# Performance work log

Hardware: AMD Instinct MI355X
Metric: run time of the kernel (lower is better)

The kernel has to match this reference:

```python
import jax, jax.numpy as jnp
import numpy as np

N, B, D_IN, UNITS, K = 8192, 1, 2, 64, 2
F = D_IN + UNITS        # concatenated feature size per node
M = K + 1               # number of diffusion matrices (x0..xK)


def setup_inputs() -> dict:
    key = jax.random.key(0)
    k1, k2, k3, k4, k5, k6 = jax.random.split(key, 6)
    inputs = jax.random.normal(k1, (B, N * D_IN), dtype=jnp.float32)
    hx = jax.random.normal(k2, (B, N * UNITS), dtype=jnp.float32)
    adj = jax.random.uniform(k3, (N, N), dtype=jnp.float32)
    w_ru = jax.random.normal(k4, (F * M, 2 * UNITS), dtype=jnp.float32) * (2.0 / (F * M + 2 * UNITS)) ** 0.5
    b_ru = jnp.ones((2 * UNITS,), dtype=jnp.float32)  # bias_start=1.0 for gates
    w_c = jax.random.normal(k5, (F * M, UNITS), dtype=jnp.float32) * (2.0 / (F * M + UNITS)) ** 0.5
    b_c = jnp.zeros((UNITS,), dtype=jnp.float32)
    node_index = jax.random.randint(k6, (N,), 0, N)
    return {"inputs": inputs, "hx": hx, "adj": adj, "w_ru": w_ru,
            "b_ru": b_ru, "w_c": w_c, "b_c": b_c, "node_index": node_index}


def _gconv(adj_mx, inp, state, W, b, out_size):
    # inp: [B, N, D_IN], state: [B, N, UNITS]
    x = jnp.concatenate([inp, state], axis=2)              # [B, N, F]
    x0 = jnp.transpose(x, (1, 2, 0)).reshape(N, F * B)     # [N, F*B]
    xs = [x0]
    x1 = adj_mx @ x0                                       # 1-hop diffusion
    xs.append(x1)
    for _ in range(2, K + 1):                              # Chebyshev-style recurrence
        x2 = 2.0 * (adj_mx @ x1) - x0
        xs.append(x2)
        x0, x1 = x1, x2
    xk = jnp.stack(xs, 0).reshape(M, N, F, B)              # [M, N, F, B]
    xk = jnp.transpose(xk, (3, 1, 2, 0)).reshape(B * N, F * M)
    out = xk @ W + b                                       # [B*N, out_size]
    return out.reshape(B, N * out_size)


def reference(inputs, hx, adj, w_ru, b_ru, w_c, b_c, node_index):
    # square adj branch: adj_mx = ((D^-1)(A+I))^T, d_mat_inv = I (unused)
    adj2 = adj + jnp.eye(N, dtype=adj.dtype)
    d_inv = 1.0 / jnp.sum(adj2, axis=1)                    # no inf: diagonal added
    adj_mx = (adj2 * d_inv[:, None]).T
    inp = inputs.reshape(B, N, D_IN)
    h3 = hx.reshape(B, N, UNITS)
    value = jax.nn.sigmoid(_gconv(adj_mx, inp, h3, w_ru, b_ru, 2 * UNITS))
    value = value.reshape(B, N, 2 * UNITS)
    r = value[..., :UNITS].reshape(B, N * UNITS)
    u = value[..., UNITS:].reshape(B, N * UNITS)
    c = jnp.tanh(_gconv(adj_mx, inp, (r * hx).reshape(B, N, UNITS), w_c, b_c, UNITS))
    new_state = u * hx + (1.0 - u) * c                     # [B, N*UNITS]
    return new_state
```

## Files before the change

### kernel.cpp

```cpp
#include <hip/hip_runtime.h>
#include <math.h>


typedef __attribute__((ext_vector_type(4))) float f32x4;
typedef __attribute__((ext_vector_type(2))) int v2i;
typedef __attribute__((ext_vector_type(4))) int v4i;
typedef unsigned char uch;

constexpr int NN  = 8192;
constexpr int CST = 80;
constexpr int KBT = 256;
constexpr int SFT = KBT / 2;
constexpr int MCH = 4;
constexpr size_t NS    = (size_t)NN * CST;
constexpr size_t UTFS8 = (size_t)SFT * 5 * 1024;

constexpr float SC1  = 4096.f,   ISC1 = 1.f / 4096.f;
constexpr float SC2  = 262144.f, ISC2 = 1.f / 262144.f;

static __device__ __forceinline__ unsigned f2e4m3(float x) {
  union { float f; unsigned u; } c; c.f = x;
  unsigned s = (c.u >> 24) & 0x80u;
  float a = fabsf(x);
  if (a >= 464.f) return s | 0x7Eu;
  if (a < 0.015625f) {
    int q = (int)(a * 512.f + 0.5f);
    return s | (unsigned)q;
  }
  c.f = a;
  unsigned u = c.u + (0x7FFFFu + ((c.u >> 20) & 1u));
  int e = (int)((u >> 23) & 0xFFu) - 127;
  unsigned m = (u >> 20) & 7u;
  if (e > 8) return s | 0x7Eu;
  return s | (unsigned)(((e + 7) << 3) | m);
}

static __device__ __forceinline__ void mfma_f8(f32x4& acc, v2i a, v2i b) {
  asm("v_mfma_f32_16x16x32_fp8_fp8 %0, %1, %2, %0" : "+v"(acc) : "v"(a), "v"(b));
}
static __device__ __forceinline__ v2i lo2(v4i v) { v2i r; r.x = v.x; r.y = v.y; return r; }
static __device__ __forceinline__ v2i hi2(v4i v) { v2i r; r.x = v.z; r.y = v.w; return r; }

__global__ __launch_bounds__(256, 4) void k_conv(const float* __restrict__ adj,
                                                 uch* __restrict__ adjF8,
                                                 float* __restrict__ dpart) {
  __shared__ float tile[2][32][132];
  const int kb = blockIdx.x, mc = blockIdx.y;
  const int tid = threadIdx.x;
  const int l = tid & 63, w = tid >> 6;
  const int rg = tid >> 5;
  const int cb = (tid & 31) * 4;
  const float* src = adj + ((size_t)kb * 32 + rg) * NN + (size_t)mc * 2048 + cb;
  float rs[4] = {0.f, 0.f, 0.f, 0.f};
  float4 vA[4], vB[4];

#pragma unroll
  for (int i = 0; i < 4; ++i)
    vA[i] = *(const float4*)(src + (size_t)(8 * i) * NN);

#define CONV_BODY(CH, BUF, VC, VN)                                             \
  {                                                                            \
    const int ch_ = (CH);                                                      \
    _Pragma("unroll") for (int i = 0; i < 4; ++i) {                            \
      int r = rg + 8 * i;                                                      \
      int colp = (cb + 8 * i) & 127;                                           \
      *(float4*)&tile[BUF][r][colp] = VC[i];                                   \
      rs[i] += (VC[i].x + VC[i].y) + (VC[i].z + VC[i].w);                      \
    }                                                                          \
    if (ch_ < 15) {                                                            \
      _Pragma("unroll") for (int i = 0; i < 4; ++i)                            \
          VN[i] = *(const float4*)(src + (size_t)(8 * i) * NN + (ch_ + 1) * 128); \
    }                                                                          \
    __syncthreads();                                                           \
    _Pragma("unroll") for (int h = 0; h < 2; ++h) {                            \
      int fl = w + 4 * h;                                                      \
      int mt = mc * 128 + ch_ * 8 + fl;                                        \
      int colp = (fl * 16 + (l & 15) + 8 * (l >> 4)) & 127;                    \
      unsigned plo = 0, phi = 0;                                               \
      _Pragma("unroll") for (int j = 0; j < 4; ++j)                            \
        plo |= f2e4m3(tile[BUF][8 * (l >> 4) + j][colp]) << (8 * j);           \
      _Pragma("unroll") for (int j = 4; j < 8; ++j)                            \
        phi |= f2e4m3(tile[BUF][8 * (l >> 4) + j][colp]) << (8 * (j - 4));     \
      uint2 pk; pk.x = plo; pk.y = phi;                                        \
      *(uint2*)(adjF8 + ((size_t)mt * SFT + (kb >> 1)) * 1024                  \
                + l * 16 + (kb & 1) * 8) = pk;                                 \
    }                                                                          \
  }

  for (int cp = 0; cp < 8; ++cp) {
    CONV_BODY(2 * cp,     0, vA, vB);
    CONV_BODY(2 * cp + 1, 1, vB, vA);
  }
#undef CONV_BODY

#pragma unroll
  for (int i = 0; i < 4; ++i) {
#pragma unroll
    for (int m = 16; m >= 1; m >>= 1) rs[i] += __shfl_xor(rs[i], m);
  }
  if ((tid & 31) == 0) {
#pragma unroll
    for (int i = 0; i < 4; ++i)
      dpart[(size_t)mc * NN + kb * 32 + 8 * i + rg] = rs[i];
  }
}

__global__ __launch_bounds__(256) void k_build(const float* __restrict__ hx,
                                               const float* __restrict__ inp,
                                               const float* __restrict__ dpart,
                                               float* __restrict__ dinv,
                                               float* __restrict__ X0,
                                               float* __restrict__ XS0,
                                               uch* __restrict__ UtF8) {
  __shared__ float dv_s[32];
  const int bid = blockIdx.x;
  const int n0 = bid * 32;
  const int tid = threadIdx.x;
  if (tid < 32) {
    int n = n0 + tid;
    float dv = 1.f / (dpart[n] + dpart[NN + n] + dpart[2 * NN + n] +
                      dpart[3 * NN + n] + 1.f);
    dv_s[tid] = dv;
    dinv[n] = dv;
  }
  __syncthreads();
  for (int p = tid; p < 32 * 20; p += 256) {
    int nl = p / 20, c4 = (p % 20) * 4;
    int n = n0 + nl;
    float dv = dv_s[nl];
    float v[4];
#pragma unroll
    for (int j = 0; j < 4; ++j) {
      int c = c4 + j;
      v[j] = (c < 64) ? hx[n * 64 + c] : (c < 66 ? inp[n * 2 + (c - 64)] : 0.f);
    }
    size_t o = (size_t)n * CST + c4;
    *(float4*)(X0 + o)  = make_float4(v[0], v[1], v[2], v[3]);
    *(float4*)(XS0 + o) = make_float4(dv * v[0], dv * v[1], dv * v[2], dv * v[3]);
  }
  for (int p = tid; p < 5 * 64; p += 256) {
    int nt = p >> 6, l = p & 63;
    unsigned plo = 0, phi = 0;
#pragma unroll
    for (int j = 0; j < 8; ++j) {
      int nloc = 8 * (l >> 4) + j;
      int n = n0 + nloc;
      int c = nt * 16 + (l & 15);
      float v = (c < 64) ? hx[n * 64 + c] : (c < 66 ? inp[n * 2 + (c - 64)] : 0.f);
      unsigned b = f2e4m3(v * dv_s[nloc] * SC1);
      if (j < 4) plo |= b << (8 * j); else phi |= b << (8 * (j - 4));
    }
    uint2 pk; pk.x = plo; pk.y = phi;
    *(uint2*)(UtF8 + ((size_t)(bid >> 1) * 5 + nt) * 1024 + l * 16 + (bid & 1) * 8) = pk;
  }
}

static __device__ __forceinline__ void gemm_core2(const uch* __restrict__ adjF8,
                                                  const uch* __restrict__ bF8,
                                                  int bid, int tid, float* smem,
                                                  float sv[5], float inv_scale) {
  const int w8 = tid >> 6, l = tid & 63;
  const int sf0 = w8 * 16;
  f32x4 acc0[5], acc1[5];
#pragma unroll
  for (int nt = 0; nt < 5; ++nt) {
    acc0[nt] = (f32x4){0.f, 0.f, 0.f, 0.f};
    acc1[nt] = (f32x4){0.f, 0.f, 0.f, 0.f};
  }
  const uch* ap = adjF8 + ((size_t)(2 * bid) * SFT + sf0) * 1024 + l * 16;
  const size_t MSTR = (size_t)SFT * 1024;
  const uch* bp = bF8 + (size_t)sf0 * 5 * 1024 + l * 16;

  v4i A0e, A1e, A0o, A1o, Be[5], Bo[5];
  A0e = *(const v4i*)(ap);
  A1e = *(const v4i*)(ap + MSTR);
#pragma unroll
  for (int nt = 0; nt < 5; ++nt) Be[nt] = *(const v4i*)(bp + nt * 1024);

  for (int sf = 0; sf < 16; sf += 2) {
    A0o = *(const v4i*)(ap + (size_t)(sf + 1) * 1024);
    A1o = *(const v4i*)(ap + MSTR + (size_t)(sf + 1) * 1024);
#pragma unroll
    for (int nt = 0; nt < 5; ++nt)
      Bo[nt] = *(const v4i*)(bp + (size_t)((sf + 1) * 5 + nt) * 1024);
#pragma unroll
    for (int nt = 0; nt < 5; ++nt) {
      mfma_f8(acc0[nt], lo2(A0e), lo2(Be[nt]));
      mfma_f8(acc1[nt], lo2(A1e), lo2(Be[nt]));
    }
#pragma unroll
    for (int nt = 0; nt < 5; ++nt) {
      mfma_f8(acc0[nt], hi2(A0e), hi2(Be[nt]));
      mfma_f8(acc1[nt], hi2(A1e), hi2(Be[nt]));
    }
    A0e = *(const v4i*)(ap + (size_t)(sf + 2) * 1024);
    A1e = *(const v4i*)(ap + MSTR + (size_t)(sf + 2) * 1024);
#pragma unroll
    for (int nt = 0; nt < 5; ++nt)
      Be[nt] = *(const v4i*)(bp + (size_t)((sf + 2) * 5 + nt) * 1024);
#pragma unroll
    for (int nt = 0; nt < 5; ++nt) {
      mfma_f8(acc0[nt], lo2(A0o), lo2(Bo[nt]));
      mfma_f8(acc1[nt], lo2(A1o), lo2(Bo[nt]));
    }
#pragma unroll
    for (int nt = 0; nt < 5; ++nt) {
      mfma_f8(acc0[nt], hi2(A0o), hi2(Bo[nt]));
      mfma_f8(acc1[nt], hi2(A1o), hi2(Bo[nt]));
    }
  }
  asm volatile("s_nop 7\n\ts_nop 7\n\ts_nop 7" ::: "memory");

  auto red = reinterpret_cast<float(*)[64][40]>(smem);
  if (w8 < 4) {
#pragma unroll
    for (int nt = 0; nt < 5; ++nt) {
      *(f32x4*)&red[w8][l][nt * 4]      = acc0[nt];
      *(f32x4*)&red[w8][l][20 + nt * 4] = acc1[nt];
    }
  }
  __syncthreads();
  if (w8 >= 4) {
#pragma unroll
    for (int nt = 0; nt < 5; ++nt) {
      f32x4 t0 = *(f32x4*)&red[w8 - 4][l][nt * 4];
      f32x4 t1 = *(f32x4*)&red[w8 - 4][l][20 + nt * 4];
      *(f32x4*)&red[w8 - 4][l][nt * 4]      = t0 + acc0[nt];
      *(f32x4*)&red[w8 - 4][l][20 + nt * 4] = t1 + acc1[nt];
    }
  }
  __syncthreads();
#pragma unroll
  for (int i = 0; i < 5; ++i) {
    int p = tid + i * 512;
    int r = p / 80, c = p % 80;
    int mtl = r >> 4, rl = r & 15;
    int ll = ((rl >> 2) << 4) | (c & 15);
    int slot = mtl * 20 + (((c >> 4) << 2) | (rl & 3));
    sv[i] = (((red[0][ll][slot] + red[1][ll][slot]) +
              red[2][ll][slot]) + red[3][ll][slot]) * inv_scale;
  }
  __syncthreads();
}

__global__ __launch_bounds__(512, 1) void k_hop1(const uch* __restrict__ adjF8,
                                                 const uch* __restrict__ UtFin,
                                                 const float* __restrict__ XSin,
                                                 const float* __restrict__ dinv,
                                                 float* __restrict__ X1,
                                                 float* __restrict__ XS1,
                                                 uch* __restrict__ UtFout) {
  __shared__ __align__(16) float smem[10240];
  const int bid = blockIdx.x, tid = threadIdx.x;
  const int n0 = bid * 32;
  float sv[5];
  gemm_core2(adjF8, UtFin, bid, tid, smem, sv, ISC1);

  auto xs = reinterpret_cast<float(*)[80]>(smem);
#pragma unroll
  for (int i = 0; i < 5; ++i) {
    int p = tid + i * 512;
    size_t o = (size_t)n0 * CST + p;
    float x1 = XSin[o] + sv[i];
    X1[o] = x1;
    float z = dinv[n0 + p / 80] * x1;
    XS1[o] = z;
    xs[p / 80][p % 80] = z;
  }
  __syncthreads();
  for (int p = tid; p < 5 * 64; p += 512) {
    int nt = p >> 6, l = p & 63;
    unsigned plo = 0, phi = 0;
#pragma unroll
    for (int j = 0; j < 8; ++j) {
      unsigned b = f2e4m3(xs[8 * (l >> 4) + j][nt * 16 + (l & 15)] * SC2);
      if (j < 4) plo |= b << (8 * j); else phi |= b << (8 * (j - 4));
    }
    uint2 pk; pk.x = plo; pk.y = phi;
    *(uint2*)(UtFout + ((size_t)(bid >> 1) * 5 + nt) * 1024 + l * 16 + (bid & 1) * 8) = pk;
  }
}

__global__ __launch_bounds__(512, 1) void k_hop2g(const uch* __restrict__ adjF8,
    const uch* __restrict__ UtFb, const float* __restrict__ XS1,
    const float* __restrict__ X0, const float* __restrict__ X1,
    const float* __restrict__ w_ru, const float* __restrict__ b_ru,
    const float* __restrict__ hx, const float* __restrict__ inp,
    const float* __restrict__ dinv,
    float* __restrict__ X0w, float* __restrict__ XS0w,
    uch* __restrict__ UtFa, float* __restrict__ UG) {
  __shared__ __align__(16) float smem[10240];
  const int bid = blockIdx.x, tid = threadIdx.x;
  const int n0 = bid * 32;
  float sv[5];
  gemm_core2(adjF8, UtFb, bid, tid, smem, sv, ISC2);

  auto xr2 = reinterpret_cast<float(*)[80]>(smem);
  float* xr01 = smem + 2560;
  float* rhq  = smem + 2560 + 4352;
#pragma unroll
  for (int i = 0; i < 5; ++i) {
    int p = tid + i * 512;
    size_t o = (size_t)n0 * CST + p;
    xr2[p / 80][p % 80] = 2.f * (XS1[o] + sv[i]) - X0[o];
  }
  for (int p = tid; p < 32 * 17; p += 512) {
    int nl = p / 17, c4 = (p % 17) * 4;
    size_t o = (size_t)(n0 + nl) * CST + c4;
    *(float4*)&xr01[nl * 68 + c4]            = *(const float4*)(X0 + o);
    *(float4*)&xr01[32 * 68 + nl * 68 + c4]  = *(const float4*)(X1 + o);
  }
  __syncthreads();

  const int nl = tid >> 4, og = tid & 15, o0 = og * 8;
  float acc[8];
#pragma unroll
  for (int j = 0; j < 8; ++j) acc[j] = b_ru[o0 + j];
  for (int c = 0; c < 66; ++c) {
    int f = (c < 64) ? (c + 2) : (c - 64);
    const float* wr = w_ru + (size_t)(f * 3) * 128 + o0;
    float xv[3];
    xv[0] = xr01[nl * 68 + c];
    xv[1] = xr01[32 * 68 + nl * 68 + c];
    xv[2] = xr2[nl][c];
#pragma unroll
    for (int m = 0; m < 3; ++m) {
      float wl[8];
      *(float4*)(wl)     = *(const float4*)(wr + m * 128);
      *(float4*)(wl + 4) = *(const float4*)(wr + m * 128 + 4);
#pragma unroll
      for (int j = 0; j < 8; ++j) acc[j] += xv[m] * wl[j];
    }
  }
  const int n = n0 + nl;
  const float dv = dinv[n];
  if (og < 8) {
#pragma unroll
    for (int j = 0; j < 8; ++j) {
      int o = o0 + j;
      float r = 1.f / (1.f + expf(-acc[j]));
      float rh = r * hx[n * 64 + o];
      X0w[(size_t)n * CST + o] = rh;
      float srh = dv * rh;
      XS0w[(size_t)n * CST + o] = srh;
      rhq[nl * 64 + o] = srh;
    }
  } else {
#pragma unroll
    for (int j = 0; j < 8; ++j)
      UG[n * 64 + (o0 - 64) + j] = 1.f / (1.f + expf(-acc[j]));
  }
  __syncthreads();
  for (int p = tid; p < 5 * 64; p += 512) {
    int nt = p >> 6, l = p & 63;
    unsigned plo = 0, phi = 0;
#pragma unroll
    for (int j = 0; j < 8; ++j) {
      int lr = 8 * (l >> 4) + j;
      int nn = n0 + lr;
      int c = nt * 16 + (l & 15);
      float v;
      if (c < 64)      v = rhq[lr * 64 + c];
      else if (c < 66) v = dinv[nn] * inp[nn * 2 + (c - 64)];
      else             v = 0.f;
      unsigned b = f2e4m3(v * SC1);
      if (j < 4) plo |= b << (8 * j); else phi |= b << (8 * (j - 4));
    }
    uint2 pk; pk.x = plo; pk.y = phi;
    *(uint2*)(UtFa + ((size_t)(bid >> 1) * 5 + nt) * 1024 + l * 16 + (bid & 1) * 8) = pk;
  }
}

__global__ __launch_bounds__(512, 1) void k_hop2f(const uch* __restrict__ adjF8,
    const uch* __restrict__ UtFb, const float* __restrict__ XS1,
    const float* __restrict__ X0, const float* __restrict__ X1,
    const float* __restrict__ w_c, const float* __restrict__ b_c,
    const float* __restrict__ hx, const float* __restrict__ UG,
    float* __restrict__ out) {
  __shared__ __align__(16) float smem[10240];
  const int bid = blockIdx.x, tid = threadIdx.x;
  const int n0 = bid * 32;
  float sv[5];
  gemm_core2(adjF8, UtFb, bid, tid, smem, sv, ISC2);

  auto xr2 = reinterpret_cast<float(*)[80]>(smem);
  float* xr01 = smem + 2560;
#pragma unroll
  for (int i = 0; i < 5; ++i) {
    int p = tid + i * 512;
    size_t o = (size_t)n0 * CST + p;
    xr2[p / 80][p % 80] = 2.f * (XS1[o] + sv[i]) - X0[o];
  }
  for (int p = tid; p < 32 * 17; p += 512) {
    int nl = p / 17, c4 = (p % 17) * 4;
    size_t o = (size_t)(n0 + nl) * CST + c4;
    *(float4*)&xr01[nl * 68 + c4]           = *(const float4*)(X0 + o);
    *(float4*)&xr01[32 * 68 + nl * 68 + c4] = *(const float4*)(X1 + o);
  }
  __syncthreads();

  const int nl = tid >> 4, ot = tid & 15, o0 = ot * 4;
  float acc[4];
#pragma unroll
  for (int j = 0; j < 4; ++j) acc[j] = b_c[o0 + j];
  for (int c = 0; c < 66; ++c) {
    int f = (c < 64) ? (c + 2) : (c - 64);
    float xv[3];
    xv[0] = xr01[nl * 68 + c];
    xv[1] = xr01[32 * 68 + nl * 68 + c];
    xv[2] = xr2[nl][c];
#pragma unroll
    for (int m = 0; m < 3; ++m) {
      float wl[4];
      *(float4*)(wl) = *(const float4*)(w_c + (size_t)(f * 3 + m) * 64 + o0);
#pragma unroll
      for (int j = 0; j < 4; ++j) acc[j] += xv[m] * wl[j];
    }
  }
  const int n = n0 + nl;
#pragma unroll
  for (int j = 0; j < 4; ++j) {
    int o = o0 + j;
    float cc = tanhf(acc[j]);
    float u = UG[n * 64 + o];
    float h = hx[n * 64 + o];
    out[n * 64 + o] = u * h + (1.f - u) * cc;
  }
}

extern "C" void kernel_launch(void* const* d_in, const int* in_sizes, int n_in,
                              void* d_out, int out_size, void* d_ws, size_t ws_size,
                              hipStream_t stream) {
  const float* inp  = (const float*)d_in[0];
  const float* hx   = (const float*)d_in[1];
  const float* adj  = (const float*)d_in[2];
  const float* w_ru = (const float*)d_in[3];
  const float* b_ru = (const float*)d_in[4];
  const float* w_c  = (const float*)d_in[5];
  const float* b_c  = (const float*)d_in[6];
  float* out = (float*)d_out;

  float* ws    = (float*)d_ws;
  float* dinv  = ws;
  float* dpart = ws + 8192;
  float* X0    = ws + 8192 + 4 * 8192;
  float* XS0   = X0 + NS;
  float* X1    = XS0 + NS;
  float* XS1   = X1 + NS;
  uch* UtFa8   = (uch*)(XS1 + NS);
  uch* UtFb8   = UtFa8 + UTFS8;
  uch* adjF8   = UtFb8 + UTFS8;
  float* UG    = (float*)(adjF8 + (size_t)512 * SFT * 1024);

  dim3 cg(KBT, MCH);

  k_conv <<<cg, 256, 0, stream>>>(adj, adjF8, dpart);
  k_build<<<NN / 32, 256, 0, stream>>>(hx, inp, dpart, dinv, X0, XS0, UtFa8);

  k_hop1 <<<256, 512, 0, stream>>>(adjF8, UtFa8, XS0, dinv, X1, XS1, UtFb8);
  k_hop2g<<<256, 512, 0, stream>>>(adjF8, UtFb8, XS1, X0, X1, w_ru, b_ru, hx, inp,
                                   dinv, X0, XS0, UtFa8, UG);

  k_hop1 <<<256, 512, 0, stream>>>(adjF8, UtFa8, XS0, dinv, X1, XS1, UtFb8);
  k_hop2f<<<256, 512, 0, stream>>>(adjF8, UtFb8, XS1, X0, X1, w_c, b_c, hx, UG, out);
}
```

Baseline: 228.5 us.

## Fuse build and hop kernels into one cooperative kernel with bf16 intermediates

Replaces the build, two hop1 and two hop2 launches with one cooperative kernel that uses grid-wide syncs between phases, which removes per-launch overhead and tail gaps. Intermediate feature matrices are stored as bf16 instead of fp32, and the scaled copies XS0/XS1 are dropped and recomputed from dinv, which cuts global memory traffic. The software fp8 conversion is replaced by the hardware packed-convert instruction. In exchange, grid.sync adds synchronisation cost, bf16 storage lowers intermediate precision, and the hardware convert may round or saturate differently.

Result: slower. 308.5 us (+35.0%).

```diff
diff --git a/kernel.cpp b/kernel.cpp
--- a/kernel.cpp
+++ b/kernel.cpp
@@ -1,11 +1,15 @@
 #include <hip/hip_runtime.h>
+#include <hip/hip_cooperative_groups.h>
 #include <math.h>
+
+namespace cg = cooperative_groups;
 
 
 typedef __attribute__((ext_vector_type(4))) float f32x4;
 typedef __attribute__((ext_vector_type(2))) int v2i;
 typedef __attribute__((ext_vector_type(4))) int v4i;
 typedef unsigned char uch;
+typedef unsigned short ush;
 
 constexpr int NN  = 8192;
 constexpr int CST = 80;
@@ -18,21 +22,26 @@
 constexpr float SC1  = 4096.f,   ISC1 = 1.f / 4096.f;
 constexpr float SC2  = 262144.f, ISC2 = 1.f / 262144.f;
 
-static __device__ __forceinline__ unsigned f2e4m3(float x) {
+static __device__ __forceinline__ float bf2f(ush u) {
+  union { float f; unsigned v; } c; c.v = ((unsigned)u) << 16; return c.f;
+}
+static __device__ __forceinline__ ush f2bf(float x) {
   union { float f; unsigned u; } c; c.f = x;
-  unsigned s = (c.u >> 24) & 0x80u;
-  float a = fabsf(x);
-  if (a >= 464.f) return s | 0x7Eu;
-  if (a < 0.015625f) {
-    int q = (int)(a * 512.f + 0.5f);
-    return s | (unsigned)q;
-  }
-  c.f = a;
-  unsigned u = c.u + (0x7FFFFu + ((c.u >> 20) & 1u));
-  int e = (int)((u >> 23) & 0xFFu) - 127;
-  unsigned m = (u >> 20) & 7u;
-  if (e > 8) return s | 0x7Eu;
-  return s | (unsigned)(((e + 7) << 3) | m);
+  unsigned u = c.u;
+  u += 0x7fffu + ((u >> 16) & 1u);
+  return (ush)(u >> 16);
+}
+
+static __device__ __forceinline__ unsigned cvt2_fp8(float a, float b) {
+  unsigned r = 0;
+  asm("v_cvt_pk_fp8_f32 %0, %1, %2" : "+v"(r) : "v"(a), "v"(b));
+  return r;
+}
+static __device__ __forceinline__ uint2 pack8_fp8(const float* tv) {
+  uint2 pk;
+  pk.x = cvt2_fp8(tv[0], tv[1]) | (cvt2_fp8(tv[2], tv[3]) << 16);
+  pk.y = cvt2_fp8(tv[4], tv[5]) | (cvt2_fp8(tv[6], tv[7]) << 16);
+  return pk;
 }
 
 static __device__ __forceinline__ void mfma_f8(f32x4& acc, v2i a, v2i b) {
@@ -76,12 +85,10 @@
       int fl = w + 4 * h;                                                      \
       int mt = mc * 128 + ch_ * 8 + fl;                                        \
       int colp = (fl * 16 + (l & 15) + 8 * (l >> 4)) & 127;                    \
-      unsigned plo = 0, phi = 0;                                               \
-      _Pragma("unroll") for (int j = 0; j < 4; ++j)                            \
-        plo |= f2e4m3(tile[BUF][8 * (l >> 4) + j][colp]) << (8 * j);           \
-      _Pragma("unroll") for (int j = 4; j < 8; ++j)                            \
-        phi |= f2e4m3(tile[BUF][8 * (l >> 4) + j][colp]) << (8 * (j - 4));     \
-      uint2 pk; pk.x = plo; pk.y = phi;                                        \
+      float tv[8];                                                             \
+      _Pragma("unroll") for (int j = 0; j < 8; ++j)                            \
+        tv[j] = tile[BUF][8 * (l >> 4) + j][colp];                             \
+      uint2 pk = pack8_fp8(tv);                                                \
       *(uint2*)(adjF8 + ((size_t)mt * SFT + (kb >> 1)) * 1024                  \
                 + l * 16 + (kb & 1) * 8) = pk;                                 \
     }                                                                          \
@@ -102,56 +109,6 @@
 #pragma unroll
     for (int i = 0; i < 4; ++i)
       dpart[(size_t)mc * NN + kb * 32 + 8 * i + rg] = rs[i];
-  }
-}
-
-__global__ __launch_bounds__(256) void k_build(const float* __restrict__ hx,
-                                               const float* __restrict__ inp,
-                                               const float* __restrict__ dpart,
-                                               float* __restrict__ dinv,
-                                               float* __restrict__ X0,
-                                               float* __restrict__ XS0,
-                                               uch* __restrict__ UtF8) {
-  __shared__ float dv_s[32];
-  const int bid = blockIdx.x;
-  const int n0 = bid * 32;
-  const int tid = threadIdx.x;
-  if (tid < 32) {
-    int n = n0 + tid;
-    float dv = 1.f / (dpart[n] + dpart[NN + n] + dpart[2 * NN + n] +
-                      dpart[3 * NN + n] + 1.f);
-    dv_s[tid] = dv;
-    dinv[n] = dv;
-  }
-  __syncthreads();
-  for (int p = tid; p < 32 * 20; p += 256) {
-    int nl = p / 20, c4 = (p % 20) * 4;
-    int n = n0 + nl;
-    float dv = dv_s[nl];
-    float v[4];
-#pragma unroll
-    for (int j = 0; j < 4; ++j) {
-      int c = c4 + j;
-      v[j] = (c < 64) ? hx[n * 64 + c] : (c < 66 ? inp[n * 2 + (c - 64)] : 0.f);
-    }
-    size_t o = (size_t)n * CST + c4;
-    *(float4*)(X0 + o)  = make_float4(v[0], v[1], v[2], v[3]);
-    *(float4*)(XS0 + o) = make_float4(dv * v[0], dv * v[1], dv * v[2], dv * v[3]);
-  }
-  for (int p = tid; p < 5 * 64; p += 256) {
-    int nt = p >> 6, l = p & 63;
-    unsigned plo = 0, phi = 0;
-#pragma unroll
-    for (int j = 0; j < 8; ++j) {
-      int nloc = 8 * (l >> 4) + j;
-      int n = n0 + nloc;
-      int c = nt * 16 + (l & 15);
-      float v = (c < 64) ? hx[n * 64 + c] : (c < 66 ? inp[n * 2 + (c - 64)] : 0.f);
-      unsigned b = f2e4m3(v * dv_s[nloc] * SC1);
-      if (j < 4) plo |= b << (8 * j); else phi |= b << (8 * (j - 4));
-    }
-    uint2 pk; pk.x = plo; pk.y = phi;
-    *(uint2*)(UtF8 + ((size_t)(bid >> 1) * 5 + nt) * 1024 + l * 16 + (bid & 1) * 8) = pk;
   }
 }
 
@@ -167,8 +124,8 @@
     acc0[nt] = (f32x4){0.f, 0.f, 0.f, 0.f};
     acc1[nt] = (f32x4){0.f, 0.f, 0.f, 0.f};
   }
+  const size_t MSTR = (size_t)SFT * 1024;
   const uch* ap = adjF8 + ((size_t)(2 * bid) * SFT + sf0) * 1024 + l * 16;
-  const size_t MSTR = (size_t)SFT * 1024;
   const uch* bp = bF8 + (size_t)sf0 * 5 * 1024 + l * 16;
 
   v4i A0e, A1e, A0o, A1o, Be[5], Bo[5];
@@ -243,188 +200,219 @@
   __syncthreads();
 }
 
-__global__ __launch_bounds__(512, 1) void k_hop1(const uch* __restrict__ adjF8,
-                                                 const uch* __restrict__ UtFin,
-                                                 const float* __restrict__ XSin,
-                                                 const float* __restrict__ dinv,
-                                                 float* __restrict__ X1,
-                                                 float* __restrict__ XS1,
-                                                 uch* __restrict__ UtFout) {
+__global__ __launch_bounds__(512, 2) void k_mega(
+    const float* __restrict__ hx, const float* __restrict__ inp,
+    const float* __restrict__ w_ru, const float* __restrict__ b_ru,
+    const float* __restrict__ w_c, const float* __restrict__ b_c,
+    float* __restrict__ out,
+    const float* __restrict__ dpart, float* __restrict__ dinv,
+    ush* __restrict__ X0b, ush* __restrict__ X1b,
+    uch* __restrict__ UtFa8, uch* __restrict__ UtFb8,
+    const uch* __restrict__ adjF8, float* __restrict__ UG) {
+  cg::grid_group grid = cg::this_grid();
   __shared__ __align__(16) float smem[10240];
-  const int bid = blockIdx.x, tid = threadIdx.x;
-  const int n0 = bid * 32;
-  float sv[5];
-  gemm_core2(adjF8, UtFin, bid, tid, smem, sv, ISC1);
-
-  auto xs = reinterpret_cast<float(*)[80]>(smem);
-#pragma unroll
-  for (int i = 0; i < 5; ++i) {
-    int p = tid + i * 512;
-    size_t o = (size_t)n0 * CST + p;
-    float x1 = XSin[o] + sv[i];
-    X1[o] = x1;
-    float z = dinv[n0 + p / 80] * x1;
-    XS1[o] = z;
-    xs[p / 80][p % 80] = z;
-  }
-  __syncthreads();
-  for (int p = tid; p < 5 * 64; p += 512) {
-    int nt = p >> 6, l = p & 63;
-    unsigned plo = 0, phi = 0;
-#pragma unroll
-    for (int j = 0; j < 8; ++j) {
-      unsigned b = f2e4m3(xs[8 * (l >> 4) + j][nt * 16 + (l & 15)] * SC2);
-      if (j < 4) plo |= b << (8 * j); else phi |= b << (8 * (j - 4));
-    }
-    uint2 pk; pk.x = plo; pk.y = phi;
-    *(uint2*)(UtFout + ((size_t)(bid >> 1) * 5 + nt) * 1024 + l * 16 + (bid & 1) * 8) = pk;
-  }
-}
-
-__global__ __launch_bounds__(512, 1) void k_hop2g(const uch* __restrict__ adjF8,
-    const uch* __restrict__ UtFb, const float* __restrict__ XS1,
-    const float* __restrict__ X0, const float* __restrict__ X1,
-    const float* __restrict__ w_ru, const float* __restrict__ b_ru,
-    const float* __restrict__ hx, const float* __restrict__ inp,
-    const float* __restrict__ dinv,
-    float* __restrict__ X0w, float* __restrict__ XS0w,
-    uch* __restrict__ UtFa, float* __restrict__ UG) {
-  __shared__ __align__(16) float smem[10240];
-  const int bid = blockIdx.x, tid = threadIdx.x;
-  const int n0 = bid * 32;
-  float sv[5];
-  gemm_core2(adjF8, UtFb, bid, tid, smem, sv, ISC2);
-
-  auto xr2 = reinterpret_cast<float(*)[80]>(smem);
-  float* xr01 = smem + 2560;
-  float* rhq  = smem + 2560 + 4352;
-#pragma unroll
-  for (int i = 0; i < 5; ++i) {
-    int p = tid + i * 512;
-    size_t o = (size_t)n0 * CST + p;
-    xr2[p / 80][p % 80] = 2.f * (XS1[o] + sv[i]) - X0[o];
-  }
-  for (int p = tid; p < 32 * 17; p += 512) {
-    int nl = p / 17, c4 = (p % 17) * 4;
-    size_t o = (size_t)(n0 + nl) * CST + c4;
-    *(float4*)&xr01[nl * 68 + c4]            = *(const float4*)(X0 + o);
-    *(float4*)&xr01[32 * 68 + nl * 68 + c4]  = *(const float4*)(X1 + o);
-  }
-  __syncthreads();
-
-  const int nl = tid >> 4, og = tid & 15, o0 = og * 8;
-  float acc[8];
-#pragma unroll
-  for (int j = 0; j < 8; ++j) acc[j] = b_ru[o0 + j];
-  for (int c = 0; c < 66; ++c) {
-    int f = (c < 64) ? (c + 2) : (c - 64);
-    const float* wr = w_ru + (size_t)(f * 3) * 128 + o0;
-    float xv[3];
-    xv[0] = xr01[nl * 68 + c];
-    xv[1] = xr01[32 * 68 + nl * 68 + c];
-    xv[2] = xr2[nl][c];
-#pragma unroll
-    for (int m = 0; m < 3; ++m) {
-      float wl[8];
-      *(float4*)(wl)     = *(const float4*)(wr + m * 128);
-      *(float4*)(wl + 4) = *(const float4*)(wr + m * 128 + 4);
-#pragma unroll
-      for (int j = 0; j < 8; ++j) acc[j] += xv[m] * wl[j];
-    }
-  }
-  const int n = n0 + nl;
-  const float dv = dinv[n];
-  if (og < 8) {
-#pragma unroll
-    for (int j = 0; j < 8; ++j) {
-      int o = o0 + j;
-      float r = 1.f / (1.f + expf(-acc[j]));
-      float rh = r * hx[n * 64 + o];
-      X0w[(size_t)n * CST + o] = rh;
-      float srh = dv * rh;
-      XS0w[(size_t)n * CST + o] = srh;
-      rhq[nl * 64 + o] = srh;
-    }
-  } else {
-#pragma unroll
-    for (int j = 0; j < 8; ++j)
-      UG[n * 64 + (o0 - 64) + j] = 1.f / (1.f + expf(-acc[j]));
-  }
-  __syncthreads();
-  for (int p = tid; p < 5 * 64; p += 512) {
-    int nt = p >> 6, l = p & 63;
-    unsigned plo = 0, phi = 0;
-#pragma unroll
-    for (int j = 0; j < 8; ++j) {
-      int lr = 8 * (l >> 4) + j;
-      int nn = n0 + lr;
-      int c = nt * 16 + (l & 15);
-      float v;
-      if (c < 64)      v = rhq[lr * 64 + c];
-      else if (c < 66) v = dinv[nn] * inp[nn * 2 + (c - 64)];
-      else             v = 0.f;
-      unsigned b = f2e4m3(v * SC1);
-      if (j < 4) plo |= b << (8 * j); else phi |= b << (8 * (j - 4));
-    }
-    uint2 pk; pk.x = plo; pk.y = phi;
-    *(uint2*)(UtFa + ((size_t)(bid >> 1) * 5 + nt) * 1024 + l * 16 + (bid & 1) * 8) = pk;
-  }
-}
-
-__global__ __launch_bounds__(512, 1) void k_hop2f(const uch* __restrict__ adjF8,
-    const uch* __restrict__ UtFb, const float* __restrict__ XS1,
-    const float* __restrict__ X0, const float* __restrict__ X1,
-    const float* __restrict__ w_c, const float* __restrict__ b_c,
-    const float* __restrict__ hx, const float* __restrict__ UG,
-    float* __restrict__ out) {
-  __shared__ __align__(16) float smem[10240];
-  const int bid = blockIdx.x, tid = threadIdx.x;
-  const int n0 = bid * 32;
-  float sv[5];
-  gemm_core2(adjF8, UtFb, bid, tid, smem, sv, ISC2);
-
-  auto xr2 = reinterpret_cast<float(*)[80]>(smem);
-  float* xr01 = smem + 2560;
-#pragma unroll
-  for (int i = 0; i < 5; ++i) {
-    int p = tid + i * 512;
-    size_t o = (size_t)n0 * CST + p;
-    xr2[p / 80][p % 80] = 2.f * (XS1[o] + sv[i]) - X0[o];
-  }
-  for (int p = tid; p < 32 * 17; p += 512) {
-    int nl = p / 17, c4 = (p % 17) * 4;
-    size_t o = (size_t)(n0 + nl) * CST + c4;
-    *(float4*)&xr01[nl * 68 + c4]           = *(const float4*)(X0 + o);
-    *(float4*)&xr01[32 * 68 + nl * 68 + c4] = *(const float4*)(X1 + o);
-  }
-  __syncthreads();
-
-  const int nl = tid >> 4, ot = tid & 15, o0 = ot * 4;
-  float acc[4];
-#pragma unroll
-  for (int j = 0; j < 4; ++j) acc[j] = b_c[o0 + j];
-  for (int c = 0; c < 66; ++c) {
-    int f = (c < 64) ? (c + 2) : (c - 64);
-    float xv[3];
-    xv[0] = xr01[nl * 68 + c];
-    xv[1] = xr01[32 * 68 + nl * 68 + c];
-    xv[2] = xr2[nl][c];
-#pragma unroll
-    for (int m = 0; m < 3; ++m) {
-      float wl[4];
-      *(float4*)(wl) = *(const float4*)(w_c + (size_t)(f * 3 + m) * 64 + o0);
-#pragma unroll
-      for (int j = 0; j < 4; ++j) acc[j] += xv[m] * wl[j];
-    }
-  }
-  const int n = n0 + nl;
-#pragma unroll
-  for (int j = 0; j < 4; ++j) {
-    int o = o0 + j;
-    float cc = tanhf(acc[j]);
-    float u = UG[n * 64 + o];
-    float h = hx[n * 64 + o];
-    out[n * 64 + o] = u * h + (1.f - u) * cc;
+  const int b = blockIdx.x, tid = threadIdx.x;
+  const int n0 = b * 32;
+
+  {
+    float* dv_s = smem;
+    if (tid < 32) {
+      int n = n0 + tid;
+      float dv = 1.f / (dpart[n] + dpart[NN + n] + dpart[2 * NN + n] +
+                        dpart[3 * NN + n] + 1.f);
+      dv_s[tid] = dv;
+      dinv[n] = dv;
+    }
+    __syncthreads();
+    for (int p = tid; p < 32 * 20; p += 512) {
+      int nl = p / 20, c4 = (p % 20) * 4;
+      int n = n0 + nl;
+      float v[4];
+#pragma unroll
+      for (int j = 0; j < 4; ++j) {
+        int c = c4 + j;
+        v[j] = (c < 64) ? hx[n * 64 + c] : (c < 66 ? inp[n * 2 + (c - 64)] : 0.f);
+      }
+      uint2 pk;
+      pk.x = f2bf(v[0]) | ((unsigned)f2bf(v[1]) << 16);
+      pk.y = f2bf(v[2]) | ((unsigned)f2bf(v[3]) << 16);
+      *(uint2*)(X0b + (size_t)n * CST + c4) = pk;
+    }
+    for (int p = tid; p < 5 * 64; p += 512) {
+      int nt = p >> 6, l = p & 63;
+      float tv[8];
+#pragma unroll
+      for (int j = 0; j < 8; ++j) {
+        int lr = 8 * (l >> 4) + j;
+        int n = n0 + lr;
+        int c = nt * 16 + (l & 15);
+        float v = (c < 64) ? hx[n * 64 + c] : (c < 66 ? inp[n * 2 + (c - 64)] : 0.f);
+        tv[j] = v * dv_s[lr] * SC1;
+      }
+      uint2 pk = pack8_fp8(tv);
+      *(uint2*)(UtFa8 + ((size_t)(b >> 1) * 5 + nt) * 1024 + l * 16 + (b & 1) * 8) = pk;
+    }
+  }
+  grid.sync();
+
+#pragma unroll 1
+  for (int round = 0; round < 2; ++round) {
+    {
+      float sv[5];
+      gemm_core2(adjF8, UtFa8, b, tid, smem, sv, ISC1);
+      auto xs = reinterpret_cast<float(*)[80]>(smem);
+#pragma unroll
+      for (int i = 0; i < 5; ++i) {
+        int p = tid + i * 512;
+        size_t o = (size_t)n0 * CST + p;
+        float dv = dinv[n0 + p / 80];
+        float x1 = dv * bf2f(X0b[o]) + sv[i];
+        X1b[o] = f2bf(x1);
+        xs[p / 80][p % 80] = dv * x1;
+      }
+      __syncthreads();
+      for (int p = tid; p < 5 * 64; p += 512) {
+        int nt = p >> 6, l = p & 63;
+        float tv[8];
+#pragma unroll
+        for (int j = 0; j < 8; ++j)
+          tv[j] = xs[8 * (l >> 4) + j][nt * 16 + (l & 15)] * SC2;
+        uint2 pk = pack8_fp8(tv);
+        *(uint2*)(UtFb8 + ((size_t)(b >> 1) * 5 + nt) * 1024 + l * 16 + (b & 1) * 8) = pk;
+      }
+    }
+    grid.sync();
+
+    if (round == 0) {
+      float sv[5];
+      gemm_core2(adjF8, UtFb8, b, tid, smem, sv, ISC2);
+      auto xr2 = reinterpret_cast<float(*)[80]>(smem);
+      float* xr01 = smem + 2560;
+      float* rhq  = smem + 2560 + 4352;
+#pragma unroll
+      for (int i = 0; i < 5; ++i) {
+        int p = tid + i * 512;
+        size_t o = (size_t)n0 * CST + p;
+        float dv = dinv[n0 + p / 80];
+        xr2[p / 80][p % 80] = 2.f * (dv * bf2f(X1b[o]) + sv[i]) - bf2f(X0b[o]);
+      }
+      for (int p = tid; p < 32 * 17; p += 512) {
+        int nl = p / 17, c4 = (p % 17) * 4;
+        size_t o = (size_t)(n0 + nl) * CST + c4;
+#pragma unroll
+        for (int j = 0; j < 4; ++j) {
+          xr01[nl * 68 + c4 + j]           = bf2f(X0b[o + j]);
+          xr01[32 * 68 + nl * 68 + c4 + j] = bf2f(X1b[o + j]);
+        }
+      }
+      __syncthreads();
+
+      const int nl = tid >> 4, og = tid & 15, o0 = og * 8;
+      float acc[8];
+#pragma unroll
+      for (int j = 0; j < 8; ++j) acc[j] = b_ru[o0 + j];
+      for (int c = 0; c < 66; ++c) {
+        int f = (c < 64) ? (c + 2) : (c - 64);
+        const float* wr = w_ru + (size_t)(f * 3) * 128 + o0;
+        float xv[3];
+        xv[0] = xr01[nl * 68 + c];
+        xv[1] = xr01[32 * 68 + nl * 68 + c];
+        xv[2] = xr2[nl][c];
+#pragma unroll
+        for (int m = 0; m < 3; ++m) {
+          float wl[8];
+          *(float4*)(wl)     = *(const float4*)(wr + m * 128);
+          *(float4*)(wl + 4) = *(const float4*)(wr + m * 128 + 4);
+#pragma unroll
+          for (int j = 0; j < 8; ++j) acc[j] += xv[m] * wl[j];
+        }
+      }
+      int n = n0 + nl;
+      float dv = dinv[n];
+      if (og < 8) {
+#pragma unroll
+        for (int j = 0; j < 8; ++j) {
+          int o = o0 + j;
+          float r = 1.f / (1.f + expf(-acc[j]));
+          float rh = r * hx[n * 64 + o];
+          X0b[(size_t)n * CST + o] = f2bf(rh);
+          rhq[nl * 64 + o] = dv * rh;
+        }
+      } else {
+#pragma unroll
+        for (int j = 0; j < 8; ++j)
+          UG[n * 64 + (o0 - 64) + j] = 1.f / (1.f + expf(-acc[j]));
+      }
+      __syncthreads();
+      for (int p = tid; p < 5 * 64; p += 512) {
+        int nt = p >> 6, l = p & 63;
+        float tv[8];
+#pragma unroll
+        for (int j = 0; j < 8; ++j) {
+          int lr = 8 * (l >> 4) + j;
+          int nn = n0 + lr;
+          int cc = nt * 16 + (l & 15);
+          float v;
+          if (cc < 64)      v = rhq[lr * 64 + cc];
+          else if (cc < 66) v = dinv[nn] * inp[nn * 2 + (cc - 64)];
+          else              v = 0.f;
+          tv[j] = v * SC1;
+        }
+        uint2 pk = pack8_fp8(tv);
+        *(uint2*)(UtFa8 + ((size_t)(b >> 1) * 5 + nt) * 1024 + l * 16 + (b & 1) * 8) = pk;
+      }
+      grid.sync();
+    } else {
+      float sv[5];
+      gemm_core2(adjF8, UtFb8, b, tid, smem, sv, ISC2);
+      auto xr2 = reinterpret_cast<float(*)[80]>(smem);
+      float* xr01 = smem + 2560;
+#pragma unroll
+      for (int i = 0; i < 5; ++i) {
+        int p = tid + i * 512;
+        size_t o = (size_t)n0 * CST + p;
+        float dv = dinv[n0 + p / 80];
+        xr2[p / 80][p % 80] = 2.f * (dv * bf2f(X1b[o]) + sv[i]) - bf2f(X0b[o]);
+      }
+      for (int p = tid; p < 32 * 17; p += 512) {
+        int nl = p / 17, c4 = (p % 17) * 4;
+        size_t o = (size_t)(n0 + nl) * CST + c4;
+#pragma unroll
+        for (int j = 0; j < 4; ++j) {
+          xr01[nl * 68 + c4 + j]           = bf2f(X0b[o + j]);
+          xr01[32 * 68 + nl * 68 + c4 + j] = bf2f(X1b[o + j]);
+        }
+      }
+      __syncthreads();
+
+      const int nl = tid >> 4, ot = tid & 15, o0 = ot * 4;
+      float acc[4];
+#pragma unroll
+      for (int j = 0; j < 4; ++j) acc[j] = b_c[o0 + j];
+      for (int c = 0; c < 66; ++c) {
+        int f = (c < 64) ? (c + 2) : (c - 64);
+        float xv[3];
+        xv[0] = xr01[nl * 68 + c];
+        xv[1] = xr01[32 * 68 + nl * 68 + c];
+        xv[2] = xr2[nl][c];
+#pragma unroll
+        for (int m = 0; m < 3; ++m) {
+          float wl[4];
+          *(float4*)(wl) = *(const float4*)(w_c + (size_t)(f * 3 + m) * 64 + o0);
+#pragma unroll
+          for (int j = 0; j < 4; ++j) acc[j] += xv[m] * wl[j];
+        }
+      }
+      int n = n0 + nl;
+#pragma unroll
+      for (int j = 0; j < 4; ++j) {
+        int o = o0 + j;
+        float cc2 = tanhf(acc[j]);
+        float u = UG[n * 64 + o];
+        float h = hx[n * 64 + o];
+        out[n * 64 + o] = u * h + (1.f - u) * cc2;
+      }
+    }
   }
 }
 
@@ -443,24 +431,19 @@
   float* ws    = (float*)d_ws;
   float* dinv  = ws;
   float* dpart = ws + 8192;
-  float* X0    = ws + 8192 + 4 * 8192;
-  float* XS0   = X0 + NS;
-  float* X1    = XS0 + NS;
-  float* XS1   = X1 + NS;
-  uch* UtFa8   = (uch*)(XS1 + NS);
+  ush* X0b     = (ush*)(ws + 8192 + 4 * 8192);
+  ush* X1b     = X0b + NS;
+  uch* UtFa8   = (uch*)(X1b + NS);
   uch* UtFb8   = UtFa8 + UTFS8;
   uch* adjF8   = UtFb8 + UTFS8;
   float* UG    = (float*)(adjF8 + (size_t)512 * SFT * 1024);
 
-  dim3 cg(KBT, MCH);
-
-  k_conv <<<cg, 256, 0, stream>>>(adj, adjF8, dpart);
-  k_build<<<NN / 32, 256, 0, stream>>>(hx, inp, dpart, dinv, X0, XS0, UtFa8);
-
-  k_hop1 <<<256, 512, 0, stream>>>(adjF8, UtFa8, XS0, dinv, X1, XS1, UtFb8);
-  k_hop2g<<<256, 512, 0, stream>>>(adjF8, UtFb8, XS1, X0, X1, w_ru, b_ru, hx, inp,
-                                   dinv, X0, XS0, UtFa8, UG);
-
-  k_hop1 <<<256, 512, 0, stream>>>(adjF8, UtFa8, XS0, dinv, X1, XS1, UtFb8);
-  k_hop2f<<<256, 512, 0, stream>>>(adjF8, UtFb8, XS1, X0, X1, w_c, b_c, hx, UG, out);
-}
+  dim3 cg2(KBT, MCH);
+  k_conv<<<cg2, 256, 0, stream>>>(adj, adjF8, dpart);
+
+  void* args[] = {(void*)&hx, (void*)&inp, (void*)&w_ru, (void*)&b_ru,
+                  (void*)&w_c, (void*)&b_c, (void*)&out, (void*)&dpart,
+                  (void*)&dinv, (void*)&X0b, (void*)&X1b, (void*)&UtFa8,
+                  (void*)&UtFb8, (void*)&adjF8, (void*)&UG};
+  hipLaunchCooperativeKernel((void*)k_mega, dim3(256), dim3(512), args, 0, stream);
+}
```
